# Kernel tuning notes

Measured on AMD Instinct MI355X. Metric: run time of the kernel, lower is better.

The kernel has to match this reference:

```python
import jax, jax.numpy as jnp
import numpy as np


def setup_inputs() -> dict:
    key = jax.random.key(0)
    k_x, k_w, k_ax, k_out = jax.random.split(key, 4)
    B, D_in = 128, 1024
    n_cores, N, A = 64, 256, 256
    n_out = 10
    pool_width = D_in + n_cores * N + 2  # inputs | all buffers | zero | one = 17410
    x = jax.random.uniform(k_x, (B, D_in), dtype=jnp.float32)  # firing probabilities
    W = jax.random.normal(k_w, (n_cores, N, A), dtype=jnp.float32)
    thresholds = jnp.ones((n_cores,), dtype=jnp.float32)
    axon_src_idx = jax.random.randint(k_ax, (n_cores, A), 0, pool_width, dtype=jnp.int32)
    out_src_idx = jax.random.randint(k_out, (n_out,), 0, pool_width, dtype=jnp.int32)
    return {"x": x, "W": W, "thresholds": thresholds,
            "axon_src_idx": axon_src_idx, "out_src_idx": out_src_idx, "cycles": 32}


def _spiking_core_flow(x, W, thresholds, axon_src_idx, out_src_idx, cycles):
    B, D_in = x.shape
    n_cores, N, A = W.shape
    thr = thresholds[:, None, None]  # [n_cores,1,1]
    dtype = x.dtype
    flat_axon = axon_src_idx.reshape(-1)

    def make_pool(spikes, buffers):
        # pool: [B, D_in + n_cores*N + 2] = inputs | buffers | zero-lane | one-lane
        buf_flat = buffers.transpose(1, 0, 2).reshape(B, n_cores * N)
        return jnp.concatenate(
            [spikes, buf_flat,
             jnp.zeros((B, 1), dtype), jnp.ones((B, 1), dtype)], axis=1)

    def step(carry, key):
        memb, buffers, out = carry
        # Bernoulli rate coding of the (flattened) input, fresh each cycle
        spikes = (jax.random.uniform(key, (B, D_in)) < x).astype(dtype)
        # gather axon signals for all cores at once: [B, n_cores, A]
        pool = make_pool(spikes, buffers)
        inp = jnp.take(pool, flat_axon, axis=1).reshape(B, n_cores, A)
        # per-core matmul: memb += input @ W^T  (batched over cores)
        memb = memb + jnp.einsum('cna,bca->cbn', W, inp)
        fired = (memb > thr).astype(dtype)          # buffers <- spikes
        memb = jnp.where(memb > thr, jnp.zeros((), dtype), memb)  # reset
        buffers = fired
        # accumulate output signals from the updated buffers
        pool2 = make_pool(spikes, buffers)
        out = out + jnp.take(pool2, out_src_idx, axis=1)
        return (memb, buffers, out), None

    memb0 = jnp.zeros((n_cores, B, N), dtype)
    buf0 = jnp.zeros((n_cores, B, N), dtype)
    out0 = jnp.zeros((B, out_src_idx.shape[0]), dtype)
    keys = jax.random.split(jax.random.key(42), cycles)
    (memb, buffers, out), _ = jax.lax.scan(step, (memb0, buf0, out0), keys)
    return out


def reference(x, W, thresholds, axon_src_idx, out_src_idx, cycles):
    return _spiking_core_flow(x, W, thresholds, axon_src_idx, out_src_idx, cycles)
```

## Files before the change

kernel.cpp:

```cpp
#include <hip/hip_runtime.h>
#include <cstdint>
#include <cstddef>


#define N_CORES   64
#define NN        256
#define AA        256
#define BB        128
#define DIN       1024
#define NOUT      10
#define CYCLES    32
#define ROW_SPK   0u
#define ROW_A     32768u
#define ROW_B     49152u
#define ROW_ZERO  65536u
#define ROW_ONE   65537u

typedef float v2f __attribute__((ext_vector_type(2)));

__device__ __forceinline__ void tf_round(uint32_t& x0, uint32_t& x1, int r) {
    x0 += x1;
    x1 = (x1 << r) | (x1 >> (32 - r));
    x1 ^= x0;
}

__device__ __forceinline__ void threefry2x32(uint32_t k0, uint32_t k1,
                                             uint32_t c0, uint32_t c1,
                                             uint32_t& o0, uint32_t& o1) {
    uint32_t ks2 = k0 ^ k1 ^ 0x1BD11BDAu;
    uint32_t x0 = c0 + k0, x1 = c1 + k1;
    tf_round(x0,x1,13); tf_round(x0,x1,15); tf_round(x0,x1,26); tf_round(x0,x1,6);
    x0 += k1; x1 += ks2 + 1u;
    tf_round(x0,x1,17); tf_round(x0,x1,29); tf_round(x0,x1,16); tf_round(x0,x1,24);
    x0 += ks2; x1 += k0 + 2u;
    tf_round(x0,x1,13); tf_round(x0,x1,15); tf_round(x0,x1,26); tf_round(x0,x1,6);
    x0 += k0; x1 += k1 + 3u;
    tf_round(x0,x1,17); tf_round(x0,x1,29); tf_round(x0,x1,16); tf_round(x0,x1,24);
    x0 += k1; x1 += ks2 + 4u;
    tf_round(x0,x1,13); tf_round(x0,x1,15); tf_round(x0,x1,26); tf_round(x0,x1,6);
    x0 += ks2; x1 += k0 + 5u;
    o0 = x0; o1 = x1;
}

__global__ void init_kernel(unsigned char* __restrict__ Pb,
                            float* __restrict__ memb,
                            float* __restrict__ out) {
    int idx = blockIdx.x * 256 + threadIdx.x;
    float4 z = {0.0f, 0.0f, 0.0f, 0.0f};
    *(float4*)(memb + (size_t)idx * 4) = z;
    *(uint32_t*)(Pb + (size_t)ROW_A * 128 + (size_t)idx * 4) = 0u;
    if (idx < 32)
        *(uint32_t*)(Pb + (size_t)ROW_ZERO * 128 + idx * 4) = 0u;
    else if (idx < 64)
        *(uint32_t*)(Pb + (size_t)ROW_ONE * 128 + (idx - 32) * 4) = 0x01010101u;
    if (idx < BB * NOUT)
        out[idx] = 0.0f;
}

__global__ void spikes_kernel(const float* __restrict__ x,
                              unsigned char* __restrict__ Pb) {
    __shared__ unsigned char S[32 * 132];
    int bx  = blockIdx.x;
    int t   = bx >> 5;
    int d0  = (bx & 31) * 32;
    int tid = threadIdx.x;

    uint32_t k0, k1;
    threefry2x32(0u, 42u, 0u, (uint32_t)t, k0, k1);

    #pragma unroll
    for (int k = 0; k < 16; ++k) {
        int e  = tid + k * 256;
        int bb = e >> 5;
        int dl = e & 31;
        int d  = d0 + dl;
        uint32_t f = (uint32_t)(bb * 1024 + d);
        uint32_t y0, y1;
        threefry2x32(k0, k1, 0u, f, y0, y1);
        uint32_t bits = y0 ^ y1;
        float u = __uint_as_float((bits >> 9) | 0x3f800000u) - 1.0f;
        S[dl * 132 + bb] = (u < x[bb * 1024 + d]) ? 1 : 0;
    }
    __syncthreads();

    int dl = tid >> 3;
    int bg = tid & 7;
    const uint32_t* Srow = (const uint32_t*)(S + dl * 132);
    uint4 v;
    v.x = Srow[bg * 4 + 0]; v.y = Srow[bg * 4 + 1];
    v.z = Srow[bg * 4 + 2]; v.w = Srow[bg * 4 + 3];
    size_t row = (size_t)t * 1024 + d0 + dl;
    *(uint4*)(Pb + row * 128 + bg * 16) = v;
}

__global__ void wt_kernel(const float* __restrict__ W, float* __restrict__ WT) {
    __shared__ float T[32][33];
    int bx = blockIdx.x;
    int c  = bx >> 6;
    int tn = (bx >> 3) & 7;
    int ta = bx & 7;
    int tid = threadIdx.x;
    int r  = tid >> 3;
    int q4 = (tid & 7) * 4;

    const float* src = W + (size_t)c * 65536 + (size_t)(tn * 32 + r) * 256 + ta * 32 + q4;
    float4 v = *(const float4*)src;
    T[r][q4 + 0] = v.x; T[r][q4 + 1] = v.y; T[r][q4 + 2] = v.z; T[r][q4 + 3] = v.w;
    __syncthreads();

    float4 o;
    o.x = T[q4 + 0][r]; o.y = T[q4 + 1][r]; o.z = T[q4 + 2][r]; o.w = T[q4 + 3][r];
    float* dst = WT + (size_t)c * 65536 + (size_t)(ta * 32 + r) * 256 + tn * 32 + q4;
    *(float4*)dst = o;
}

__global__ void offtab_kernel(const int* __restrict__ axon,
                              const int* __restrict__ outsrc,
                              uint32_t* __restrict__ off_tab,
                              uint32_t* __restrict__ out_off) {
    int bx = blockIdx.x;
    int tid = threadIdx.x;
    if (bx < 2048) {
        int idx = bx * 256 + tid;
        int t   = idx >> 14;
        int ca  = idx & 16383;
        int j   = axon[ca];
        uint32_t row;
        if (j < 1024)        row = (uint32_t)(t * 1024 + j);
        else if (j < 17408)  row = (((t & 1) == 0) ? ROW_A : ROW_B) + (uint32_t)(j - 1024);
        else                 row = (j == 17408) ? ROW_ZERO : ROW_ONE;
        off_tab[idx] = row * 128u;
    } else {
        for (int idx = tid; idx < CYCLES * NOUT; idx += 256) {
            int t = idx / NOUT, o = idx % NOUT;
            int j = outsrc[o];
            uint32_t row;
            if (j < 1024)        row = (uint32_t)(t * 1024 + j);
            else if (j < 17408)  row = (((t & 1) == 0) ? ROW_B : ROW_A) + (uint32_t)(j - 1024);
            else                 row = (j == 17408) ? ROW_ZERO : ROW_ONE;
            out_off[idx] = row * 128u;
        }
    }
}

#define MF_ST 20

__global__ __launch_bounds__(256, 2) void core_kernel(
    const unsigned char* __restrict__ Pb,
    unsigned char* __restrict__ Pw,
    const float* __restrict__ WT,
    const uint32_t* __restrict__ off_t,
    float* __restrict__ memb,
    const float* __restrict__ thresholds,
    uint32_t wbyte_base,
    const uint32_t* __restrict__ out_off_prev,
    float* __restrict__ d_out,
    int do_out)
{
    __shared__ float Mf[256 * MF_ST];

    int tid = threadIdx.x;
    int bx  = blockIdx.x;

    if (do_out && bx == 0 && tid < BB) {
        #pragma unroll
        for (int o = 0; o < NOUT; ++o) {
            uint32_t off = out_off_prev[o];
            d_out[tid * NOUT + o] += (float)Pb[off + (uint32_t)tid];
        }
    }

    int c     = (bx & 7) * 8 + ((bx >> 3) & 7);
    int bg    = bx >> 6;
    int b0blk = bg * 16;

    {
        uint32_t off = off_t[c * 256 + tid];
        uint4 v = *(const uint4*)(Pb + off + (uint32_t)b0blk);
        const unsigned char* pb = (const unsigned char*)&v;
        float* dst = Mf + tid * MF_ST;
        #pragma unroll
        for (int q = 0; q < 4; ++q) {
            float4 f;
            f.x = (float)pb[4 * q + 0];
            f.y = (float)pb[4 * q + 1];
            f.z = (float)pb[4 * q + 2];
            f.w = (float)pb[4 * q + 3];
            *(float4*)(dst + 4 * q) = f;
        }
    }
    __syncthreads();

    int lane = tid & 63;
    int wid  = __builtin_amdgcn_readfirstlane(tid >> 6);
    int bo   = wid & 1;
    int nh   = wid >> 1;
    int b0   = b0blk + bo * 8;
    int n0   = nh * 128;

    const float* wt   = WT + (size_t)c * 65536 + n0 + lane * 2;
    const float* mrow = Mf + bo * 8;

    v2f acc0[4], acc1[4];
    #pragma unroll
    for (int bp = 0; bp < 4; ++bp) { acc0[bp] = (v2f){0.f, 0.f}; acc1[bp] = (v2f){0.f, 0.f}; }

    #pragma unroll 4
    for (int a = 0; a < 256; ++a) {
        v2f w = *(const v2f*)(wt + (size_t)a * 256);
        float4 mlo = *(const float4*)(mrow + a * MF_ST);
        float4 mhi = *(const float4*)(mrow + a * MF_ST + 4);
        v2f m0 = {mlo.x, mlo.y};
        v2f m1 = {mlo.z, mlo.w};
        v2f m2 = {mhi.x, mhi.y};
        v2f m3 = {mhi.z, mhi.w};
        v2f w0 = {w.x, w.x};
        v2f w1 = {w.y, w.y};
        acc0[0] = __builtin_elementwise_fma(w0, m0, acc0[0]);
        acc0[1] = __builtin_elementwise_fma(w0, m1, acc0[1]);
        acc0[2] = __builtin_elementwise_fma(w0, m2, acc0[2]);
        acc0[3] = __builtin_elementwise_fma(w0, m3, acc0[3]);
        acc1[0] = __builtin_elementwise_fma(w1, m0, acc1[0]);
        acc1[1] = __builtin_elementwise_fma(w1, m1, acc1[1]);
        acc1[2] = __builtin_elementwise_fma(w1, m2, acc1[2]);
        acc1[3] = __builtin_elementwise_fma(w1, m3, acc1[3]);
    }

    float thr = thresholds[c];
    #pragma unroll
    for (int nj = 0; nj < 2; ++nj) {
        int n = n0 + 2 * lane + nj;
        size_t rowb = (size_t)(c * 256 + n) * 128 + b0;
        const v2f* accp = (nj == 0) ? acc0 : acc1;
        float4 m0 = *(const float4*)(memb + rowb);
        float4 m1 = *(const float4*)(memb + rowb + 4);
        float vv[8];
        vv[0] = m0.x + accp[0].x;  vv[1] = m0.y + accp[0].y;
        vv[2] = m0.z + accp[1].x;  vv[3] = m0.w + accp[1].y;
        vv[4] = m1.x + accp[2].x;  vv[5] = m1.y + accp[2].y;
        vv[6] = m1.z + accp[3].x;  vv[7] = m1.w + accp[3].y;
        uint32_t flo = 0, fhi = 0;
        float st[8];
        #pragma unroll
        for (int k = 0; k < 8; ++k) {
            bool f = vv[k] > thr;
            st[k] = f ? 0.0f : vv[k];
            if (k < 4) flo |= (f ? 1u : 0u) << (8 * k);
            else       fhi |= (f ? 1u : 0u) << (8 * (k - 4));
        }
        float4 s0 = {st[0], st[1], st[2], st[3]};
        float4 s1 = {st[4], st[5], st[6], st[7]};
        *(float4*)(memb + rowb)     = s0;
        *(float4*)(memb + rowb + 4) = s1;
        uint2 fb = {flo, fhi};
        *(uint2*)(Pw + wbyte_base + rowb) = fb;
    }
}

__global__ void tail_kernel(const unsigned char* __restrict__ Pb,
                            const uint32_t* __restrict__ out_off31,
                            float* __restrict__ d_out) {
    int tid = threadIdx.x;
    if (tid < BB) {
        #pragma unroll
        for (int o = 0; o < NOUT; ++o) {
            uint32_t off = out_off31[o];
            d_out[tid * NOUT + o] += (float)Pb[off + (uint32_t)tid];
        }
    }
}

extern "C" void kernel_launch(void* const* d_in, const int* in_sizes, int n_in,
                              void* d_out_, int out_size, void* d_ws, size_t ws_size,
                              hipStream_t stream) {
    const float* x          = (const float*)d_in[0];
    const float* W          = (const float*)d_in[1];
    const float* thresholds = (const float*)d_in[2];
    const int*   axon       = (const int*)d_in[3];
    const int*   outsrc     = (const int*)d_in[4];

    if (ws_size < (size_t)45 * 1024 * 1024) return;

    unsigned char* ws      = (unsigned char*)d_ws;
    unsigned char* Pb      = ws;
    float*         WT      = (float*)(ws + (size_t)(16u << 20));
    uint32_t*      off_tab = (uint32_t*)(ws + (size_t)(32u << 20));
    uint32_t*      out_off = (uint32_t*)(ws + (size_t)(32u << 20) + 2u * 1024u * 1024u);
    float*         memb    = (float*)(ws + (size_t)(36u << 20));
    float*         out     = (float*)d_out_;

    init_kernel<<<2048, 256, 0, stream>>>(Pb, memb, out);
    spikes_kernel<<<1024, 256, 0, stream>>>(x, Pb);
    wt_kernel<<<4096, 256, 0, stream>>>(W, WT);
    offtab_kernel<<<2049, 256, 0, stream>>>(axon, outsrc, off_tab, out_off);

    for (int t = 0; t < CYCLES; ++t) {
        uint32_t wrow = ((t & 1) == 0) ? ROW_B : ROW_A;
        const uint32_t* oprev = out_off + (t > 0 ? (t - 1) * NOUT : 0);
        core_kernel<<<512, 256, 0, stream>>>(
            Pb, Pb, WT, off_tab + (size_t)t * 16384, memb, thresholds,
            wrow * 128u, oprev, out, t > 0 ? 1 : 0);
    }
    tail_kernel<<<1, 128, 0, stream>>>(Pb, out_off + 31 * NOUT, out);
}
```

Measured before the change: 752.1 us.

## Pack spike inputs into bitmasks in LDS and double-buffer weight loads

```diff
diff --git a/kernel.cpp b/kernel.cpp
--- a/kernel.cpp
+++ b/kernel.cpp
@@ -143,8 +143,6 @@
     }
 }
 
-#define MF_ST 20
-
 __global__ __launch_bounds__(256, 2) void core_kernel(
     const unsigned char* __restrict__ Pb,
     unsigned char* __restrict__ Pw,
@@ -157,7 +155,7 @@
     float* __restrict__ d_out,
     int do_out)
 {
-    __shared__ float Mf[256 * MF_ST];
+    __shared__ uint32_t MW[2][64];
 
     int tid = threadIdx.x;
     int bx  = blockIdx.x;
@@ -178,16 +176,14 @@
         uint32_t off = off_t[c * 256 + tid];
         uint4 v = *(const uint4*)(Pb + off + (uint32_t)b0blk);
         const unsigned char* pb = (const unsigned char*)&v;
-        float* dst = Mf + tid * MF_ST;
+        uint32_t lo = 0, hi = 0;
         #pragma unroll
-        for (int q = 0; q < 4; ++q) {
-            float4 f;
-            f.x = (float)pb[4 * q + 0];
-            f.y = (float)pb[4 * q + 1];
-            f.z = (float)pb[4 * q + 2];
-            f.w = (float)pb[4 * q + 3];
-            *(float4*)(dst + 4 * q) = f;
-        }
+        for (int j = 0; j < 8; ++j) {
+            lo |= (uint32_t)(pb[j] & 1u) << j;
+            hi |= (uint32_t)(pb[8 + j] & 1u) << j;
+        }
+        ((unsigned char*)MW[0])[tid] = (unsigned char)lo;
+        ((unsigned char*)MW[1])[tid] = (unsigned char)hi;
     }
     __syncthreads();
 
@@ -198,33 +194,60 @@
     int b0   = b0blk + bo * 8;
     int n0   = nh * 128;
 
-    const float* wt   = WT + (size_t)c * 65536 + n0 + lane * 2;
-    const float* mrow = Mf + bo * 8;
+    const float* wt = WT + (size_t)c * 65536 + n0 + lane * 2;
+    const uint32_t* mwp = MW[bo];
 
     v2f acc0[4], acc1[4];
     #pragma unroll
     for (int bp = 0; bp < 4; ++bp) { acc0[bp] = (v2f){0.f, 0.f}; acc1[bp] = (v2f){0.f, 0.f}; }
 
-    #pragma unroll 4
-    for (int a = 0; a < 256; ++a) {
-        v2f w = *(const v2f*)(wt + (size_t)a * 256);
-        float4 mlo = *(const float4*)(mrow + a * MF_ST);
-        float4 mhi = *(const float4*)(mrow + a * MF_ST + 4);
-        v2f m0 = {mlo.x, mlo.y};
-        v2f m1 = {mlo.z, mlo.w};
-        v2f m2 = {mhi.x, mhi.y};
-        v2f m3 = {mhi.z, mhi.w};
-        v2f w0 = {w.x, w.x};
-        v2f w1 = {w.y, w.y};
-        acc0[0] = __builtin_elementwise_fma(w0, m0, acc0[0]);
-        acc0[1] = __builtin_elementwise_fma(w0, m1, acc0[1]);
-        acc0[2] = __builtin_elementwise_fma(w0, m2, acc0[2]);
-        acc0[3] = __builtin_elementwise_fma(w0, m3, acc0[3]);
-        acc1[0] = __builtin_elementwise_fma(w1, m0, acc1[0]);
-        acc1[1] = __builtin_elementwise_fma(w1, m1, acc1[1]);
-        acc1[2] = __builtin_elementwise_fma(w1, m2, acc1[2]);
-        acc1[3] = __builtin_elementwise_fma(w1, m3, acc1[3]);
-    }
+    v2f wA[8], wB[8];
+    uint32_t bAlo, bAhi, bBlo, bBhi;
+
+#define LOADW(Wb, ch)                                                         \
+    { const float* p_ = wt + (size_t)(ch) * 8 * 256;                          \
+      _Pragma("unroll")                                                       \
+      for (int i_ = 0; i_ < 8; ++i_)                                          \
+          Wb[i_] = *(const v2f*)(p_ + (size_t)i_ * 256); }
+
+#define RDBITS(lo_, hi_, ch)                                                  \
+    { uint2 t_ = *(const uint2*)(mwp + (ch) * 2);                             \
+      lo_ = (uint32_t)__builtin_amdgcn_readfirstlane((int)t_.x);              \
+      hi_ = (uint32_t)__builtin_amdgcn_readfirstlane((int)t_.y); }
+
+#define FMACH(Wb, blo_, bhi_)                                                 \
+    { _Pragma("unroll")                                                       \
+      for (int i_ = 0; i_ < 8; ++i_) {                                        \
+          uint32_t byt_ = (((i_ < 4) ? (blo_) : (bhi_)) >> (8 * (i_ & 3))) & 0xFFu; \
+          v2f w_  = Wb[i_];                                                   \
+          v2f w0_ = {w_.x, w_.x};                                             \
+          v2f w1_ = {w_.y, w_.y};                                             \
+          _Pragma("unroll")                                                   \
+          for (int bp_ = 0; bp_ < 4; ++bp_) {                                 \
+              uint32_t m0_ = (0u - ((byt_ >> (2 * bp_)) & 1u)) & 0x3F800000u; \
+              uint32_t m1_ = (0u - ((byt_ >> (2 * bp_ + 1)) & 1u)) & 0x3F800000u; \
+              v2f m2_ = __builtin_bit_cast(v2f,                               \
+                          ((uint64_t)m1_ << 32) | (uint64_t)m0_);             \
+              acc0[bp_] = __builtin_elementwise_fma(w0_, m2_, acc0[bp_]);     \
+              acc1[bp_] = __builtin_elementwise_fma(w1_, m2_, acc1[bp_]);     \
+          }                                                                   \
+      } }
+
+    RDBITS(bAlo, bAhi, 0);
+    LOADW(wA, 0);
+    for (int ch = 0; ch < 32; ch += 2) {
+        RDBITS(bBlo, bBhi, ch + 1);
+        LOADW(wB, ch + 1);
+        FMACH(wA, bAlo, bAhi);
+        if (ch + 2 < 32) {
+            RDBITS(bAlo, bAhi, ch + 2);
+            LOADW(wA, ch + 2);
+        }
+        FMACH(wB, bBlo, bBhi);
+    }
+#undef LOADW
+#undef RDBITS
+#undef FMACH
 
     float thr = thresholds[c];
     #pragma unroll
```

After: 1.167 ms. 1.55x slower.
